# Optimization experiments

Measured on AMD Instinct MI355X. Metric: run time of the kernel, lower is better.

The kernel has to match this reference:

```python
import jax, jax.numpy as jnp
import numpy as np

MAX_LEN = 64  # global max_len in the original code


def _lstm_cell(h, c, x_t, Wih, Whh, bih, bhh):
    # torch LSTM gate order: i, f, g, o ; Wih/Whh are [4H, H]
    gates = x_t @ Wih.T + h @ Whh.T + bih + bhh  # [B, 4H]
    i, f, g, o = jnp.split(gates, 4, axis=-1)
    c_new = jax.nn.sigmoid(f) * c + jax.nn.sigmoid(i) * jnp.tanh(g)
    h_new = jax.nn.sigmoid(o) * jnp.tanh(c_new)
    return h_new, c_new


def setup_inputs() -> dict:
    V, H, B, S = 32000, 512, 32, 64
    key = jax.random.key(0)
    ks = jax.random.split(key, 12)
    sc_x = 1.0 / np.sqrt(H)
    inp = {
        "x": jax.random.randint(ks[0], (B, S), 0, V, dtype=jnp.int32),
        "emb": jax.random.normal(ks[1], (V, H), dtype=jnp.float32) * 0.02,
        "enc_Wih": jax.random.normal(ks[2], (4 * H, H), dtype=jnp.float32) * sc_x,
        "enc_Whh": jax.random.normal(ks[3], (4 * H, H), dtype=jnp.float32) * sc_x,
        "enc_bih": jnp.zeros((4 * H,), dtype=jnp.float32),
        "enc_bhh": jnp.zeros((4 * H,), dtype=jnp.float32),
        "dec_Wih": jax.random.normal(ks[4], (4 * H, H), dtype=jnp.float32) * sc_x,
        "dec_Whh": jax.random.normal(ks[5], (4 * H, H), dtype=jnp.float32) * sc_x,
        "dec_bih": jnp.zeros((4 * H,), dtype=jnp.float32),
        "dec_bhh": jnp.zeros((4 * H,), dtype=jnp.float32),
        "W_out": jax.random.normal(ks[6], (V, H), dtype=jnp.float32) * sc_x,
        "b_out": jnp.zeros((V,), dtype=jnp.float32),
        "dec_sos": 1,
    }
    return inp


def reference(x, emb, enc_Wih, enc_Whh, enc_bih, enc_bhh,
              dec_Wih, dec_Whh, dec_bih, dec_bhh, W_out, b_out, dec_sos):
    B, S = x.shape
    H = emb.shape[1]

    # ----- Encoder: LSTM over [B, S, H] embedded input -----
    x_emb = emb[x]  # [B, S, H]

    def enc_step(carry, e_t):
        h, c = carry
        h, c = _lstm_cell(h, c, e_t, enc_Wih, enc_Whh, enc_bih, enc_bhh)
        return (h, c), h

    h0 = jnp.zeros((B, H), dtype=emb.dtype)
    c0 = jnp.zeros((B, H), dtype=emb.dtype)
    (h_enc, c_enc), enc_out = jax.lax.scan(enc_step, (h0, c0),
                                           jnp.swapaxes(x_emb, 0, 1))
    enc_out = jnp.swapaxes(enc_out, 0, 1)  # [B, S, H]

    # ----- Greedy decode loop: emb -> LSTM step -> linear -> log_softmax -> argmax -----
    tok0 = jnp.full((B,), dec_sos, dtype=x.dtype)

    def dec_step(carry, _):
        h, c, tok = carry
        e = emb[tok]  # [B, H]
        h, c = _lstm_cell(h, c, e, dec_Wih, dec_Whh, dec_bih, dec_bhh)
        logp = jax.nn.log_softmax(h @ W_out.T + b_out, axis=-1)  # [B, V]
        nxt = jnp.argmax(logp, axis=-1).astype(x.dtype)  # topk(1) index
        return (h, c, nxt), (nxt, logp)

    (_, _, _), (toks, logps) = jax.lax.scan(
        dec_step, (h_enc, c_enc, tok0), None, length=MAX_LEN)

    out1 = jnp.swapaxes(toks, 0, 1)   # [B, MAX_LEN] greedy token ids
    out2 = jnp.swapaxes(logps, 0, 1)  # [B, MAX_LEN, V] log-probs (squeezed)
    return out1, out2, enc_out
```

## Files before the change

kernel.cpp:

```cpp
#include <hip/hip_runtime.h>
#include <math.h>

#define VOC 32000
#define HID 512
#define BAT 32
#define SEQ 64

#define B_EIHT 0u
#define B_EHHT 4194304u
#define B_DIHT 8388608u
#define B_DHHT 12582912u
#define B_XD   16777216u
#define B_H    33554432u
#define B_C    33685504u
#define B_E    33816576u
#define B_GT   33882112u
#define B_LG   34144256u
#define B_PM   38240256u
#define B_PS   38305792u
#define B_PK   38371328u
#define B_M    38502400u
#define B_LS   38502528u
#define B_TK   38502656u

#define OUT_TOK  0u
#define OUT_LOGP 2048u
#define OUT_ENC  65538048u

__device__ __forceinline__ unsigned long long packkey(float x, int v) {
    unsigned int fb = __float_as_uint(x);
    unsigned int key = (fb & 0x80000000u) ? ~fb : (fb | 0x80000000u);
    return ((unsigned long long)key << 32) | (unsigned int)(~(unsigned int)v);
}
__device__ __forceinline__ float sigf(float x) { return 1.0f / (1.0f + expf(-x)); }

__global__ void k_tr(const float* __restrict__ src, float* __restrict__ dst) {
    __shared__ float lds[32][33];
    int c0 = blockIdx.x * 32, r0 = blockIdx.y * 32;
    int cl = threadIdx.x & 31, r8 = threadIdx.x >> 5;
    for (int rr = 0; rr < 4; ++rr) {
        int r = r8 + rr * 8;
        lds[r][cl] = src[(size_t)(r0 + r) * HID + c0 + cl];
    }
    __syncthreads();
    for (int rr = 0; rr < 4; ++rr) {
        int idx = threadIdx.x + rr * 256;
        int rl = idx & 31, c2 = idx >> 5;
        dst[(size_t)(c0 + c2) * 2048 + r0 + rl] = lds[rl][c2];
    }
}

__global__ void k_zero(char* __restrict__ ws) {
    int i = blockIdx.x * 256 + threadIdx.x;
    ((float*)(ws + B_H))[i] = 0.f;
    ((float*)(ws + B_C))[i] = 0.f;
}

__global__ void __launch_bounds__(256) k_xd(const int* __restrict__ x, const float* __restrict__ emb,
                                            char* __restrict__ ws) {
    __shared__ float e_s[512];
    int r = blockIdx.x;
    int j4 = blockIdx.y * 256 + threadIdx.x;
    const float* erow = emb + (size_t)x[r] * HID;
    for (int k = threadIdx.x; k < HID; k += 256) e_s[k] = erow[k];
    __syncthreads();
    const float* WT = (const float*)(ws + B_EIHT);
    float acc = 0.f;
    for (int k = 0; k < HID; ++k)
        acc = fmaf(WT[(size_t)k * 2048 + j4], e_s[k], acc);
    ((float*)(ws + B_XD))[(size_t)r * 2048 + j4] = acc;
}

__global__ void __launch_bounds__(256) k_gates(const float* __restrict__ bih,
                                               const float* __restrict__ bhh,
                                               const float* __restrict__ Hin,
                                               char* __restrict__ ws, int t, int mode) {
    __shared__ float h_s[512];
    __shared__ float e_s[512];
    int b = blockIdx.x & 31, jb = blockIdx.x >> 5;
    int j4 = jb * 256 + threadIdx.x;
    for (int k = threadIdx.x; k < HID; k += 256) {
        h_s[k] = Hin[b * HID + k];
        if (mode == 1) e_s[k] = ((const float*)(ws + B_E))[b * HID + k];
    }
    __syncthreads();
    float xd;
    if (mode == 0) {
        xd = ((const float*)(ws + B_XD))[(size_t)(b * SEQ + t) * 2048 + j4];
    } else {
        const float* WT = (const float*)(ws + B_DIHT);
        float a = 0.f;
        for (int k = 0; k < HID; ++k)
            a = fmaf(WT[(size_t)k * 2048 + j4], e_s[k], a);
        xd = a;
    }
    const float* WH = (const float*)(ws + (mode == 0 ? B_EHHT : B_DHHT));
    float hd = 0.f;
    for (int k = 0; k < HID; ++k)
        hd = fmaf(WH[(size_t)k * 2048 + j4], h_s[k], hd);
    float g = (xd + hd) + bih[j4];
    g = g + bhh[j4];
    ((float*)(ws + B_GT))[b * 2048 + j4] = g;
}

__global__ void k_cell(char* __restrict__ ws,
                       const float* __restrict__ Cin,
                       float* __restrict__ Hout, float* __restrict__ Cout,
                       float* __restrict__ dout, int t, int mode) {
    int i = blockIdx.x * 256 + threadIdx.x;
    int b = i >> 9, j = i & 511;
    const float* gb = (const float*)(ws + B_GT) + b * 2048;
    float ip = sigf(gb[j]);
    float fp = sigf(gb[512 + j]);
    float gp = tanhf(gb[1024 + j]);
    float op = sigf(gb[1536 + j]);
    float cn = fp * Cin[i] + ip * gp;
    float hn = op * tanhf(cn);
    Hout[i] = hn;
    Cout[i] = cn;
    if (mode == 0)
        dout[OUT_ENC + (size_t)b * (SEQ * HID) + (size_t)t * HID + j] = hn;
}

__global__ void k_embt(const int* __restrict__ sos, const float* __restrict__ emb,
                       char* __restrict__ ws, int t) {
    int b = blockIdx.x;
    int tok = (t == 0) ? sos[0] : ((const int*)(ws + B_TK))[b];
    const float* erow = emb + (size_t)tok * HID;
    for (int k = threadIdx.x; k < HID; k += 256)
        ((float*)(ws + B_E))[b * HID + k] = erow[k];
}

__global__ void __launch_bounds__(256) k_logits(const float* __restrict__ Hin,
                                                const float* __restrict__ Wout,
                                                const float* __restrict__ bout,
                                                char* __restrict__ ws) {
    __shared__ float h2[16][512];
    int vb = blockIdx.x, bh = blockIdx.y;
    for (int i = threadIdx.x; i < 16 * 512; i += 256) {
        int bb = i >> 9, k = i & 511;
        h2[bb][k] = Hin[(bh * 16 + bb) * HID + k];
    }
    __syncthreads();
    int v = vb * 256 + threadIdx.x;
    const float* wr = Wout + (size_t)v * HID;
    float acc[16];
#pragma unroll
    for (int i = 0; i < 16; ++i) acc[i] = 0.f;
    for (int k = 0; k < HID; k += 4) {
        float4 w = *(const float4*)&wr[k];
#pragma unroll
        for (int bb = 0; bb < 16; ++bb) {
            float4 h4 = *(const float4*)&h2[bb][k];
            float a = acc[bb];
            a = fmaf(w.x, h4.x, a);
            a = fmaf(w.y, h4.y, a);
            a = fmaf(w.z, h4.z, a);
            a = fmaf(w.w, h4.w, a);
            acc[bb] = a;
        }
    }
    float bq = bout[v];
    float mx[16];
#pragma unroll
    for (int bb = 0; bb < 16; ++bb) {
        float lg = acc[bb] + bq;
        ((float*)(ws + B_LG))[(size_t)(bh * 16 + bb) * VOC + v] = lg;
        mx[bb] = lg;
    }
#pragma unroll
    for (int m = 1; m < 64; m <<= 1)
#pragma unroll
        for (int bb = 0; bb < 16; ++bb) mx[bb] = fmaxf(mx[bb], __shfl_xor(mx[bb], m));
    if ((threadIdx.x & 63) == 0) {
        int col = vb * 4 + (threadIdx.x >> 6);
#pragma unroll
        for (int bb = 0; bb < 16; ++bb)
            ((float*)(ws + B_PM))[(bh * 16 + bb) * 512 + col] = mx[bb];
    }
}

__global__ void k_finM(char* __restrict__ ws) {
    __shared__ float sh[4];
    int b = blockIdx.x;
    float m = -3.4e38f;
    for (int c = threadIdx.x; c < 500; c += 256)
        m = fmaxf(m, ((const float*)(ws + B_PM))[b * 512 + c]);
#pragma unroll
    for (int k = 1; k < 64; k <<= 1) m = fmaxf(m, __shfl_xor(m, k));
    if ((threadIdx.x & 63) == 0) sh[threadIdx.x >> 6] = m;
    __syncthreads();
    if (threadIdx.x == 0)
        ((float*)(ws + B_M))[b] = fmaxf(fmaxf(sh[0], sh[1]), fmaxf(sh[2], sh[3]));
}

__global__ void __launch_bounds__(256) k_passB(char* __restrict__ ws) {
    int vb = blockIdx.x, bg = blockIdx.y;
    int b0 = bg * 2;
    int v = vb * 256 + threadIdx.x;
    float e2[2];
#pragma unroll
    for (int row = 0; row < 2; ++row) {
        int b = b0 + row;
        float m = ((const float*)(ws + B_M))[b];
        float* p = (float*)(ws + B_LG) + (size_t)b * VOC + v;
        float sv = *p - m;
        *p = sv;
        e2[row] = expf(sv);
    }
#pragma unroll
    for (int m = 1; m < 64; m <<= 1) {
        e2[0] += __shfl_xor(e2[0], m);
        e2[1] += __shfl_xor(e2[1], m);
    }
    if ((threadIdx.x & 63) == 0) {
        int col = vb * 4 + (threadIdx.x >> 6);
        ((float*)(ws + B_PS))[b0 * 512 + col] = e2[0];
        ((float*)(ws + B_PS))[(b0 + 1) * 512 + col] = e2[1];
    }
}

__global__ void k_finS(char* __restrict__ ws) {
    __shared__ float sh[4];
    int b = blockIdx.x;
    float s = 0.f;
    for (int c = threadIdx.x; c < 500; c += 256)
        s += ((const float*)(ws + B_PS))[b * 512 + c];
#pragma unroll
    for (int k = 1; k < 64; k <<= 1) s += __shfl_xor(s, k);
    if ((threadIdx.x & 63) == 0) sh[threadIdx.x >> 6] = s;
    __syncthreads();
    if (threadIdx.x == 0)
        ((float*)(ws + B_LS))[b] = logf(sh[0] + sh[1] + sh[2] + sh[3]);
}

__global__ void __launch_bounds__(256) k_passC(char* __restrict__ ws, float* __restrict__ dout, int t) {
    int vb = blockIdx.x, bg = blockIdx.y;
    int b0 = bg * 2;
    int v = vb * 256 + threadIdx.x;
    unsigned long long pk2[2];
#pragma unroll
    for (int row = 0; row < 2; ++row) {
        int b = b0 + row;
        float L = ((const float*)(ws + B_LS))[b];
        float sv = ((const float*)(ws + B_LG))[(size_t)b * VOC + v];
        float lp = sv - L;
        dout[OUT_LOGP + (size_t)(b * SEQ + t) * VOC + v] = lp;
        pk2[row] = packkey(lp, v);
    }
#pragma unroll
    for (int m = 1; m < 64; m <<= 1) {
#pragma unroll
        for (int row = 0; row < 2; ++row) {
            unsigned long long o = __shfl_xor(pk2[row], m);
            if (o > pk2[row]) pk2[row] = o;
        }
    }
    if ((threadIdx.x & 63) == 0) {
        int col = vb * 4 + (threadIdx.x >> 6);
        ((unsigned long long*)(ws + B_PK))[b0 * 512 + col] = pk2[0];
        ((unsigned long long*)(ws + B_PK))[(b0 + 1) * 512 + col] = pk2[1];
    }
}

__global__ void k_finT(char* __restrict__ ws, float* __restrict__ dout, int t) {
    __shared__ unsigned long long sh[4];
    int b = blockIdx.x;
    unsigned long long pk = 0ull;
    for (int c = threadIdx.x; c < 500; c += 256) {
        unsigned long long o = ((const unsigned long long*)(ws + B_PK))[b * 512 + c];
        if (o > pk) pk = o;
    }
#pragma unroll
    for (int k = 1; k < 64; k <<= 1) {
        unsigned long long o = __shfl_xor(pk, k);
        if (o > pk) pk = o;
    }
    if ((threadIdx.x & 63) == 0) sh[threadIdx.x >> 6] = pk;
    __syncthreads();
    if (threadIdx.x == 0) {
        pk = sh[0];
        if (sh[1] > pk) pk = sh[1];
        if (sh[2] > pk) pk = sh[2];
        if (sh[3] > pk) pk = sh[3];
        int v = (int)(~(unsigned)(pk & 0xFFFFFFFFull));
        ((int*)(ws + B_TK))[b] = v;
        dout[OUT_TOK + b * SEQ + t] = (float)v;
    }
}

extern "C" void kernel_launch(void* const* d_in, const int* in_sizes, int n_in,
                              void* d_out, int out_size, void* d_ws, size_t ws_size,
                              hipStream_t stream) {
    const int*   x    = (const int*)d_in[0];
    const float* emb  = (const float*)d_in[1];
    const float* eWih = (const float*)d_in[2];
    const float* eWhh = (const float*)d_in[3];
    const float* ebih = (const float*)d_in[4];
    const float* ebhh = (const float*)d_in[5];
    const float* dWih = (const float*)d_in[6];
    const float* dWhh = (const float*)d_in[7];
    const float* dbih = (const float*)d_in[8];
    const float* dbhh = (const float*)d_in[9];
    const float* Wout = (const float*)d_in[10];
    const float* bout = (const float*)d_in[11];
    const int*   sos  = (const int*)d_in[12];
    float* out = (float*)d_out;
    char*  ws  = (char*)d_ws;

    float* H = (float*)(ws + B_H);
    float* C = (float*)(ws + B_C);

    hipLaunchKernelGGL(k_tr, dim3(16, 64), dim3(256), 0, stream, eWih, (float*)(ws + B_EIHT));
    hipLaunchKernelGGL(k_tr, dim3(16, 64), dim3(256), 0, stream, eWhh, (float*)(ws + B_EHHT));
    hipLaunchKernelGGL(k_tr, dim3(16, 64), dim3(256), 0, stream, dWih, (float*)(ws + B_DIHT));
    hipLaunchKernelGGL(k_tr, dim3(16, 64), dim3(256), 0, stream, dWhh, (float*)(ws + B_DHHT));
    hipLaunchKernelGGL(k_xd, dim3(2048, 8), dim3(256), 0, stream, x, emb, ws);
    hipLaunchKernelGGL(k_zero, dim3(64), dim3(256), 0, stream, ws);

    for (int t = 0; t < SEQ; ++t) {
        int pi = t & 1, po = pi ^ 1;
        hipLaunchKernelGGL(k_gates, dim3(256), dim3(256), 0, stream,
                           ebih, ebhh, H + pi * 16384, ws, t, 0);
        hipLaunchKernelGGL(k_cell, dim3(64), dim3(256), 0, stream,
                           ws, C + pi * 16384, H + po * 16384, C + po * 16384, out, t, 0);
    }
    for (int t = 0; t < SEQ; ++t) {
        int pi = t & 1, po = pi ^ 1;
        hipLaunchKernelGGL(k_embt, dim3(32), dim3(256), 0, stream, sos, emb, ws, t);
        hipLaunchKernelGGL(k_gates, dim3(256), dim3(256), 0, stream,
                           dbih, dbhh, H + pi * 16384, ws, t, 1);
        hipLaunchKernelGGL(k_cell, dim3(64), dim3(256), 0, stream,
                           ws, C + pi * 16384, H + po * 16384, C + po * 16384, out, t, 1);
        hipLaunchKernelGGL(k_logits, dim3(125, 2), dim3(256), 0, stream,
                           H + po * 16384, Wout, bout, ws);
        hipLaunchKernelGGL(k_finM, dim3(32), dim3(256), 0, stream, ws);
        hipLaunchKernelGGL(k_passB, dim3(125, 16), dim3(256), 0, stream, ws);
        hipLaunchKernelGGL(k_finS, dim3(32), dim3(256), 0, stream, ws);
        hipLaunchKernelGGL(k_passC, dim3(125, 16), dim3(256), 0, stream, ws, out, t);
        hipLaunchKernelGGL(k_finT, dim3(32), dim3(256), 0, stream, ws, out, t);
    }
}
```

Measured before the change: 9.202 ms.

## Fuse LSTM gates with cell update, merge softmax passes, batch input projection

```diff
diff --git a/kernel.cpp b/kernel.cpp
--- a/kernel.cpp
+++ b/kernel.cpp
@@ -10,18 +10,13 @@
 #define B_EHHT 4194304u
 #define B_DIHT 8388608u
 #define B_DHHT 12582912u
-#define B_XD   16777216u
-#define B_H    33554432u
-#define B_C    33685504u
-#define B_E    33816576u
-#define B_GT   33882112u
-#define B_LG   34144256u
-#define B_PM   38240256u
-#define B_PS   38305792u
-#define B_PK   38371328u
-#define B_M    38502400u
-#define B_LS   38502528u
-#define B_TK   38502656u
+#define B_E2   16777216u
+#define B_XD   20971520u
+#define B_H    37748736u
+#define B_C    37879808u
+#define B_LG   38010880u
+#define B_PM   42106880u
+#define B_TK   42172416u
 
 #define OUT_TOK  0u
 #define OUT_LOGP 2048u
@@ -34,7 +29,7 @@
 }
 __device__ __forceinline__ float sigf(float x) { return 1.0f / (1.0f + expf(-x)); }
 
-__global__ void k_tr(const float* __restrict__ src, float* __restrict__ dst) {
+__global__ void k_trg(const float* __restrict__ src, float* __restrict__ dst) {
     __shared__ float lds[32][33];
     int c0 = blockIdx.x * 32, r0 = blockIdx.y * 32;
     int cl = threadIdx.x & 31, r8 = threadIdx.x >> 5;
@@ -46,8 +41,40 @@
     for (int rr = 0; rr < 4; ++rr) {
         int idx = threadIdx.x + rr * 256;
         int rl = idx & 31, c2 = idx >> 5;
-        dst[(size_t)(c0 + c2) * 2048 + r0 + rl] = lds[rl][c2];
-    }
+        int row = r0 + rl;
+        int p = ((row & 511) << 2) | (row >> 9);
+        dst[(size_t)(c0 + c2) * 2048 + p] = lds[rl][c2];
+    }
+}
+
+__global__ void k_gather(const int* __restrict__ x, const float* __restrict__ emb,
+                         char* __restrict__ ws) {
+    int r = blockIdx.x;
+    const float* erow = emb + (size_t)x[r] * HID;
+    float* e2 = (float*)(ws + B_E2) + (size_t)r * HID;
+    e2[threadIdx.x] = erow[threadIdx.x];
+    e2[threadIdx.x + 256] = erow[threadIdx.x + 256];
+}
+
+__global__ void __launch_bounds__(256) k_xd2(char* __restrict__ ws) {
+    int rt = blockIdx.x;
+    int jc = blockIdx.y;
+    int p = jc * 256 + threadIdx.x;
+    const float* WT = (const float*)(ws + B_EIHT);
+    const float* E2 = (const float*)(ws + B_E2) + (size_t)rt * 16 * HID;
+    float acc[16];
+#pragma unroll
+    for (int i = 0; i < 16; ++i) acc[i] = 0.f;
+    for (int k = 0; k < HID; ++k) {
+        float w = WT[(size_t)k * 2048 + p];
+#pragma unroll
+        for (int rr = 0; rr < 16; ++rr)
+            acc[rr] = fmaf(w, E2[rr * HID + k], acc[rr]);
+    }
+    float* XD = (float*)(ws + B_XD);
+#pragma unroll
+    for (int rr = 0; rr < 16; ++rr)
+        XD[(size_t)(rt * 16 + rr) * 2048 + p] = acc[rr];
 }
 
 __global__ void k_zero(char* __restrict__ ws) {
@@ -56,102 +83,81 @@
     ((float*)(ws + B_C))[i] = 0.f;
 }
 
-__global__ void __launch_bounds__(256) k_xd(const int* __restrict__ x, const float* __restrict__ emb,
-                                            char* __restrict__ ws) {
+__global__ void __launch_bounds__(256) k_step(const float* __restrict__ bih,
+                                              const float* __restrict__ bhh,
+                                              const float* __restrict__ emb,
+                                              const int* __restrict__ sos,
+                                              const float* __restrict__ Hin,
+                                              const float* __restrict__ Cin,
+                                              float* __restrict__ Hout,
+                                              float* __restrict__ Cout,
+                                              char* __restrict__ ws,
+                                              float* __restrict__ dout,
+                                              int t, int mode) {
     __shared__ float e_s[512];
-    int r = blockIdx.x;
-    int j4 = blockIdx.y * 256 + threadIdx.x;
-    const float* erow = emb + (size_t)x[r] * HID;
-    for (int k = threadIdx.x; k < HID; k += 256) e_s[k] = erow[k];
-    __syncthreads();
-    const float* WT = (const float*)(ws + B_EIHT);
-    float acc = 0.f;
-    for (int k = 0; k < HID; ++k)
-        acc = fmaf(WT[(size_t)k * 2048 + j4], e_s[k], acc);
-    ((float*)(ws + B_XD))[(size_t)r * 2048 + j4] = acc;
-}
-
-__global__ void __launch_bounds__(256) k_gates(const float* __restrict__ bih,
-                                               const float* __restrict__ bhh,
-                                               const float* __restrict__ Hin,
-                                               char* __restrict__ ws, int t, int mode) {
-    __shared__ float h_s[512];
-    __shared__ float e_s[512];
-    int b = blockIdx.x & 31, jb = blockIdx.x >> 5;
-    int j4 = jb * 256 + threadIdx.x;
-    for (int k = threadIdx.x; k < HID; k += 256) {
-        h_s[k] = Hin[b * HID + k];
-        if (mode == 1) e_s[k] = ((const float*)(ws + B_E))[b * HID + k];
-    }
-    __syncthreads();
-    float xd;
-    if (mode == 0) {
-        xd = ((const float*)(ws + B_XD))[(size_t)(b * SEQ + t) * 2048 + j4];
+    __shared__ float gsh[256];
+    int b = blockIdx.x >> 3, jc = blockIdx.x & 7;
+    int p = jc * 256 + threadIdx.x;
+    const float* hb = Hin + b * HID;
+    float g;
+    int oj = ((p & 3) << 9) | (p >> 2);
+    if (mode == 1) {
+        int tok = (t == 0) ? sos[0] : ((const int*)(ws + B_TK))[b];
+        const float* erow = emb + (size_t)tok * HID;
+        e_s[threadIdx.x] = erow[threadIdx.x];
+        e_s[threadIdx.x + 256] = erow[threadIdx.x + 256];
+        __syncthreads();
+        const float* WI = (const float*)(ws + B_DIHT);
+        const float* WH = (const float*)(ws + B_DHHT);
+        float aI = 0.f, aH = 0.f;
+        for (int k = 0; k < HID; ++k) {
+            aI = fmaf(WI[(size_t)k * 2048 + p], e_s[k], aI);
+            aH = fmaf(WH[(size_t)k * 2048 + p], hb[k], aH);
+        }
+        g = (aI + aH) + bih[oj];
+        g = g + bhh[oj];
     } else {
-        const float* WT = (const float*)(ws + B_DIHT);
-        float a = 0.f;
+        const float* WH = (const float*)(ws + B_EHHT);
+        float aH = 0.f;
         for (int k = 0; k < HID; ++k)
-            a = fmaf(WT[(size_t)k * 2048 + j4], e_s[k], a);
-        xd = a;
-    }
-    const float* WH = (const float*)(ws + (mode == 0 ? B_EHHT : B_DHHT));
-    float hd = 0.f;
-    for (int k = 0; k < HID; ++k)
-        hd = fmaf(WH[(size_t)k * 2048 + j4], h_s[k], hd);
-    float g = (xd + hd) + bih[j4];
-    g = g + bhh[j4];
-    ((float*)(ws + B_GT))[b * 2048 + j4] = g;
-}
-
-__global__ void k_cell(char* __restrict__ ws,
-                       const float* __restrict__ Cin,
-                       float* __restrict__ Hout, float* __restrict__ Cout,
-                       float* __restrict__ dout, int t, int mode) {
-    int i = blockIdx.x * 256 + threadIdx.x;
-    int b = i >> 9, j = i & 511;
-    const float* gb = (const float*)(ws + B_GT) + b * 2048;
-    float ip = sigf(gb[j]);
-    float fp = sigf(gb[512 + j]);
-    float gp = tanhf(gb[1024 + j]);
-    float op = sigf(gb[1536 + j]);
-    float cn = fp * Cin[i] + ip * gp;
-    float hn = op * tanhf(cn);
-    Hout[i] = hn;
-    Cout[i] = cn;
-    if (mode == 0)
-        dout[OUT_ENC + (size_t)b * (SEQ * HID) + (size_t)t * HID + j] = hn;
-}
-
-__global__ void k_embt(const int* __restrict__ sos, const float* __restrict__ emb,
-                       char* __restrict__ ws, int t) {
-    int b = blockIdx.x;
-    int tok = (t == 0) ? sos[0] : ((const int*)(ws + B_TK))[b];
-    const float* erow = emb + (size_t)tok * HID;
-    for (int k = threadIdx.x; k < HID; k += 256)
-        ((float*)(ws + B_E))[b * HID + k] = erow[k];
+            aH = fmaf(WH[(size_t)k * 2048 + p], hb[k], aH);
+        float xd = ((const float*)(ws + B_XD))[(size_t)(b * SEQ + t) * 2048 + p];
+        g = (xd + aH) + bih[oj];
+        g = g + bhh[oj];
+    }
+    gsh[threadIdx.x] = g;
+    __syncthreads();
+    if (threadIdx.x < 64) {
+        int j = jc * 64 + threadIdx.x;
+        float gi = gsh[threadIdx.x * 4 + 0];
+        float gf = gsh[threadIdx.x * 4 + 1];
+        float gg = gsh[threadIdx.x * 4 + 2];
+        float go = gsh[threadIdx.x * 4 + 3];
+        float ip = sigf(gi), fp = sigf(gf), gp = tanhf(gg), op = sigf(go);
+        float cn = __fadd_rn(__fmul_rn(fp, Cin[b * HID + j]), __fmul_rn(ip, gp));
+        float hn = __fmul_rn(op, tanhf(cn));
+        Hout[b * HID + j] = hn;
+        Cout[b * HID + j] = cn;
+        if (mode == 0)
+            dout[OUT_ENC + (size_t)b * (SEQ * HID) + (size_t)t * HID + j] = hn;
+    }
 }
 
 __global__ void __launch_bounds__(256) k_logits(const float* __restrict__ Hin,
                                                 const float* __restrict__ Wout,
                                                 const float* __restrict__ bout,
                                                 char* __restrict__ ws) {
-    __shared__ float h2[16][512];
-    int vb = blockIdx.x, bh = blockIdx.y;
-    for (int i = threadIdx.x; i < 16 * 512; i += 256) {
-        int bb = i >> 9, k = i & 511;
-        h2[bb][k] = Hin[(bh * 16 + bb) * HID + k];
-    }
-    __syncthreads();
+    int vb = blockIdx.x;
     int v = vb * 256 + threadIdx.x;
     const float* wr = Wout + (size_t)v * HID;
-    float acc[16];
-#pragma unroll
-    for (int i = 0; i < 16; ++i) acc[i] = 0.f;
+    float acc[32];
+#pragma unroll
+    for (int i = 0; i < 32; ++i) acc[i] = 0.f;
     for (int k = 0; k < HID; k += 4) {
         float4 w = *(const float4*)&wr[k];
 #pragma unroll
-        for (int bb = 0; bb < 16; ++bb) {
-            float4 h4 = *(const float4*)&h2[bb][k];
+        for (int bb = 0; bb < 32; ++bb) {
+            float4 h4 = *(const float4*)&Hin[(size_t)bb * HID + k];
             float a = acc[bb];
             a = fmaf(w.x, h4.x, a);
             a = fmaf(w.y, h4.y, a);
@@ -161,114 +167,63 @@
         }
     }
     float bq = bout[v];
-    float mx[16];
-#pragma unroll
-    for (int bb = 0; bb < 16; ++bb) {
+    float* LG = (float*)(ws + B_LG);
+    float mx[32];
+#pragma unroll
+    for (int bb = 0; bb < 32; ++bb) {
         float lg = acc[bb] + bq;
-        ((float*)(ws + B_LG))[(size_t)(bh * 16 + bb) * VOC + v] = lg;
+        LG[(size_t)bb * VOC + v] = lg;
         mx[bb] = lg;
     }
 #pragma unroll
     for (int m = 1; m < 64; m <<= 1)
 #pragma unroll
-        for (int bb = 0; bb < 16; ++bb) mx[bb] = fmaxf(mx[bb], __shfl_xor(mx[bb], m));
+        for (int bb = 0; bb < 32; ++bb) mx[bb] = fmaxf(mx[bb], __shfl_xor(mx[bb], m));
     if ((threadIdx.x & 63) == 0) {
         int col = vb * 4 + (threadIdx.x >> 6);
 #pragma unroll
-        for (int bb = 0; bb < 16; ++bb)
-            ((float*)(ws + B_PM))[(bh * 16 + bb) * 512 + col] = mx[bb];
-    }
-}
-
-__global__ void k_finM(char* __restrict__ ws) {
-    __shared__ float sh[4];
+        for (int bb = 0; bb < 32; ++bb)
+            ((float*)(ws + B_PM))[bb * 512 + col] = mx[bb];
+    }
+}
+
+__global__ void __launch_bounds__(256) k_soft(char* __restrict__ ws, float* __restrict__ dout, int t) {
+    __shared__ float ps_sh[512];
+    __shared__ float msh[4], ssh[4];
+    __shared__ unsigned long long pksh[4];
     int b = blockIdx.x;
+    int tid = threadIdx.x, lane = tid & 63, wv = tid >> 6;
+    const float* pm = (const float*)(ws + B_PM) + b * 512;
     float m = -3.4e38f;
-    for (int c = threadIdx.x; c < 500; c += 256)
-        m = fmaxf(m, ((const float*)(ws + B_PM))[b * 512 + c]);
+    for (int c = tid; c < 500; c += 256) m = fmaxf(m, pm[c]);
 #pragma unroll
     for (int k = 1; k < 64; k <<= 1) m = fmaxf(m, __shfl_xor(m, k));
-    if ((threadIdx.x & 63) == 0) sh[threadIdx.x >> 6] = m;
-    __syncthreads();
-    if (threadIdx.x == 0)
-        ((float*)(ws + B_M))[b] = fmaxf(fmaxf(sh[0], sh[1]), fmaxf(sh[2], sh[3]));
-}
-
-__global__ void __launch_bounds__(256) k_passB(char* __restrict__ ws) {
-    int vb = blockIdx.x, bg = blockIdx.y;
-    int b0 = bg * 2;
-    int v = vb * 256 + threadIdx.x;
-    float e2[2];
-#pragma unroll
-    for (int row = 0; row < 2; ++row) {
-        int b = b0 + row;
-        float m = ((const float*)(ws + B_M))[b];
-        float* p = (float*)(ws + B_LG) + (size_t)b * VOC + v;
-        float sv = *p - m;
-        *p = sv;
-        e2[row] = expf(sv);
-    }
-#pragma unroll
-    for (int m = 1; m < 64; m <<= 1) {
-        e2[0] += __shfl_xor(e2[0], m);
-        e2[1] += __shfl_xor(e2[1], m);
-    }
-    if ((threadIdx.x & 63) == 0) {
-        int col = vb * 4 + (threadIdx.x >> 6);
-        ((float*)(ws + B_PS))[b0 * 512 + col] = e2[0];
-        ((float*)(ws + B_PS))[(b0 + 1) * 512 + col] = e2[1];
-    }
-}
-
-__global__ void k_finS(char* __restrict__ ws) {
-    __shared__ float sh[4];
-    int b = blockIdx.x;
+    if (lane == 0) msh[wv] = m;
+    __syncthreads();
+    float M = fmaxf(fmaxf(msh[0], msh[1]), fmaxf(msh[2], msh[3]));
+    float* lg = (float*)(ws + B_LG) + (size_t)b * VOC;
+    for (int c = wv; c < 500; c += 4) {
+        float sv = lg[c * 64 + lane] - M;
+        lg[c * 64 + lane] = sv;
+        float e = expf(sv);
+#pragma unroll
+        for (int k = 1; k < 64; k <<= 1) e += __shfl_xor(e, k);
+        if (lane == 0) ps_sh[c] = e;
+    }
+    __syncthreads();
     float s = 0.f;
-    for (int c = threadIdx.x; c < 500; c += 256)
-        s += ((const float*)(ws + B_PS))[b * 512 + c];
+    for (int c = tid; c < 500; c += 256) s += ps_sh[c];
 #pragma unroll
     for (int k = 1; k < 64; k <<= 1) s += __shfl_xor(s, k);
-    if ((threadIdx.x & 63) == 0) sh[threadIdx.x >> 6] = s;
-    __syncthreads();
-    if (threadIdx.x == 0)
-        ((float*)(ws + B_LS))[b] = logf(sh[0] + sh[1] + sh[2] + sh[3]);
-}
-
-__global__ void __launch_bounds__(256) k_passC(char* __restrict__ ws, float* __restrict__ dout, int t) {
-    int vb = blockIdx.x, bg = blockIdx.y;
-    int b0 = bg * 2;
-    int v = vb * 256 + threadIdx.x;
-    unsigned long long pk2[2];
-#pragma unroll
-    for (int row = 0; row < 2; ++row) {
-        int b = b0 + row;
-        float L = ((const float*)(ws + B_LS))[b];
-        float sv = ((const float*)(ws + B_LG))[(size_t)b * VOC + v];
-        float lp = sv - L;
-        dout[OUT_LOGP + (size_t)(b * SEQ + t) * VOC + v] = lp;
-        pk2[row] = packkey(lp, v);
-    }
-#pragma unroll
-    for (int m = 1; m < 64; m <<= 1) {
-#pragma unroll
-        for (int row = 0; row < 2; ++row) {
-            unsigned long long o = __shfl_xor(pk2[row], m);
-            if (o > pk2[row]) pk2[row] = o;
-        }
-    }
-    if ((threadIdx.x & 63) == 0) {
-        int col = vb * 4 + (threadIdx.x >> 6);
-        ((unsigned long long*)(ws + B_PK))[b0 * 512 + col] = pk2[0];
-        ((unsigned long long*)(ws + B_PK))[(b0 + 1) * 512 + col] = pk2[1];
-    }
-}
-
-__global__ void k_finT(char* __restrict__ ws, float* __restrict__ dout, int t) {
-    __shared__ unsigned long long sh[4];
-    int b = blockIdx.x;
+    if (lane == 0) ssh[wv] = s;
+    __syncthreads();
+    float L = logf(((ssh[0] + ssh[1]) + ssh[2]) + ssh[3]);
+    float* outrow = dout + OUT_LOGP + (size_t)(b * SEQ + t) * VOC;
     unsigned long long pk = 0ull;
-    for (int c = threadIdx.x; c < 500; c += 256) {
-        unsigned long long o = ((const unsigned long long*)(ws + B_PK))[b * 512 + c];
+    for (int i = tid; i < VOC; i += 256) {
+        float lp = lg[i] - L;
+        outrow[i] = lp;
+        unsigned long long o = packkey(lp, i);
         if (o > pk) pk = o;
     }
 #pragma unroll
@@ -276,13 +231,13 @@
         unsigned long long o = __shfl_xor(pk, k);
         if (o > pk) pk = o;
     }
-    if ((threadIdx.x & 63) == 0) sh[threadIdx.x >> 6] = pk;
-    __syncthreads();
-    if (threadIdx.x == 0) {
-        pk = sh[0];
-        if (sh[1] > pk) pk = sh[1];
-        if (sh[2] > pk) pk = sh[2];
-        if (sh[3] > pk) pk = sh[3];
+    if (lane == 0) pksh[wv] = pk;
+    __syncthreads();
+    if (tid == 0) {
+        pk = pksh[0];
+        if (pksh[1] > pk) pk = pksh[1];
+        if (pksh[2] > pk) pk = pksh[2];
+        if (pksh[3] > pk) pk = pksh[3];
         int v = (int)(~(unsigned)(pk & 0xFFFFFFFFull));
         ((int*)(ws + B_TK))[b] = v;
         dout[OUT_TOK + b * SEQ + t] = (float)v;
@@ -311,33 +266,27 @@
     float* H = (float*)(ws + B_H);
     float* C = (float*)(ws + B_C);
 
-    hipLaunchKernelGGL(k_tr, dim3(16, 64), dim3(256), 0, stream, eWih, (float*)(ws + B_EIHT));
-    hipLaunchKernelGGL(k_tr, dim3(16, 64), dim3(256), 0, stream, eWhh, (float*)(ws + B_EHHT));
-    hipLaunchKernelGGL(k_tr, dim3(16, 64), dim3(256), 0, stream, dWih, (float*)(ws + B_DIHT));
-    hipLaunchKernelGGL(k_tr, dim3(16, 64), dim3(256), 0, stream, dWhh, (float*)(ws + B_DHHT));
-    hipLaunchKernelGGL(k_xd, dim3(2048, 8), dim3(256), 0, stream, x, emb, ws);
+    hipLaunchKernelGGL(k_trg, dim3(16, 64), dim3(256), 0, stream, eWih, (float*)(ws + B_EIHT));
+    hipLaunchKernelGGL(k_trg, dim3(16, 64), dim3(256), 0, stream, eWhh, (float*)(ws + B_EHHT));
+    hipLaunchKernelGGL(k_trg, dim3(16, 64), dim3(256), 0, stream, dWih, (float*)(ws + B_DIHT));
+    hipLaunchKernelGGL(k_trg, dim3(16, 64), dim3(256), 0, stream, dWhh, (float*)(ws + B_DHHT));
+    hipLaunchKernelGGL(k_gather, dim3(2048), dim3(256), 0, stream, x, emb, ws);
+    hipLaunchKernelGGL(k_xd2, dim3(128, 8), dim3(256), 0, stream, ws);
     hipLaunchKernelGGL(k_zero, dim3(64), dim3(256), 0, stream, ws);
 
     for (int t = 0; t < SEQ; ++t) {
         int pi = t & 1, po = pi ^ 1;
-        hipLaunchKernelGGL(k_gates, dim3(256), dim3(256), 0, stream,
-                           ebih, ebhh, H + pi * 16384, ws, t, 0);
-        hipLaunchKernelGGL(k_cell, dim3(64), dim3(256), 0, stream,
-                           ws, C + pi * 16384, H + po * 16384, C + po * 16384, out, t, 0);
+        hipLaunchKernelGGL(k_step, dim3(256), dim3(256), 0, stream,
+                           ebih, ebhh, emb, sos, H + pi * 16384, C + pi * 16384,
+                           H + po * 16384, C + po * 16384, ws, out, t, 0);
     }
     for (int t = 0; t < SEQ; ++t) {
         int pi = t & 1, po = pi ^ 1;
-        hipLaunchKernelGGL(k_embt, dim3(32), dim3(256), 0, stream, sos, emb, ws, t);
-        hipLaunchKernelGGL(k_gates, dim3(256), dim3(256), 0, stream,
-                           dbih, dbhh, H + pi * 16384, ws, t, 1);
-        hipLaunchKernelGGL(k_cell, dim3(64), dim3(256), 0, stream,
-                           ws, C + pi * 16384, H + po * 16384, C + po * 16384, out, t, 1);
-        hipLaunchKernelGGL(k_logits, dim3(125, 2), dim3(256), 0, stream,
+        hipLaunchKernelGGL(k_step, dim3(256), dim3(256), 0, stream,
+                           dbih, dbhh, emb, sos, H + pi * 16384, C + pi * 16384,
+                           H + po * 16384, C + po * 16384, ws, out, t, 1);
+        hipLaunchKernelGGL(k_logits, dim3(125), dim3(256), 0, stream,
                            H + po * 16384, Wout, bout, ws);
-        hipLaunchKernelGGL(k_finM, dim3(32), dim3(256), 0, stream, ws);
-        hipLaunchKernelGGL(k_passB, dim3(125, 16), dim3(256), 0, stream, ws);
-        hipLaunchKernelGGL(k_finS, dim3(32), dim3(256), 0, stream, ws);
-        hipLaunchKernelGGL(k_passC, dim3(125, 16), dim3(256), 0, stream, ws, out, t);
-        hipLaunchKernelGGL(k_finT, dim3(32), dim3(256), 0, stream, ws, out, t);
-    }
-}
+        hipLaunchKernelGGL(k_soft, dim3(32), dim3(256), 0, stream, ws, out, t);
+    }
+}
```

After: 18.16 ms. 97.3% more time.
